# Performance work log

Hardware: AMD Instinct MI355X
Metric: run time of the kernel (lower is better)

Reference implementation:

```python
import jax, jax.numpy as jnp
import numpy as np


def setup_inputs() -> dict:
    key = jax.random.key(0)
    k1, k2 = jax.random.split(key)
    inputs = jax.random.normal(k1, (64, 16, 64, 512), dtype=jnp.float32)
    cluster_centers = jax.random.normal(k2, (64, 512), dtype=jnp.float32) * 0.05
    return {"inputs": inputs, "cluster_centers": cluster_centers}


def reference(inputs, cluster_centers):
    # inputs: (B, H, W, C); cluster_centers: (K, C)
    B, H, W, C = inputs.shape
    K = cluster_centers.shape[0]
    x = inputs.reshape(B, H * W, C)                      # (B, N, C)
    # soft assignments: softmax over K of x @ centers^T
    logits = jnp.einsum('bnc,kc->bnk', x, cluster_centers)
    a = jax.nn.softmax(logits, axis=-1)                  # (B, N, K)
    # VLAD rewritten to avoid (B,N,K,C) residual tensor:
    # sum_n a[b,n,k] * (x[b,n,:] - c[k,:])
    #   = (a^T @ x)[b,k,:] - (sum_n a[b,n,k]) * c[k,:]
    agg = jnp.einsum('bnk,bnc->bkc', a, x)               # (B, K, C)
    a_sum = jnp.sum(a, axis=1)                           # (B, K)
    vlad = agg - a_sum[:, :, None] * cluster_centers[None, :, :]
    vlad = vlad.reshape(B, K * C)
    # tf.nn.l2_normalize: x / sqrt(max(sum(x^2), eps)), eps=1e-12
    norm = jnp.sqrt(jnp.maximum(jnp.sum(vlad * vlad, axis=-1, keepdims=True), 1e-12))
    return vlad / norm
```

## Files before the change

### kernel.cpp

```cpp
#include <hip/hip_runtime.h>
#include <stdint.h>

#define NB 64
#define NN 1024
#define CDIM 512
#define KK 64
#define RS 72

typedef __attribute__((ext_vector_type(4))) float f32x4;
typedef __attribute__((ext_vector_type(8))) short short8;
typedef __attribute__((ext_vector_type(4))) unsigned short u16x4;

__device__ __forceinline__ unsigned short f2bf(float f) {
  unsigned int u = __float_as_uint(f);
  return (unsigned short)((u + 0x7fffu + ((u >> 16) & 1u)) >> 16);
}

__global__ __launch_bounds__(256) void k0_cvt(const float* __restrict__ cc,
                                              unsigned short* __restrict__ ccb) {
  int i = blockIdx.x * 256 + threadIdx.x;
  ccb[i] = f2bf(cc[i]);
}

__global__ __launch_bounds__(256) void k1_assign(const float* __restrict__ x,
    const unsigned short* __restrict__ ccb, unsigned short* __restrict__ a_t,
    float* __restrict__ a_sum) {
  const int b = blockIdx.y;
  const int n0 = blockIdx.x << 6;
  const int tid = threadIdx.x;
  const int w = tid >> 6;
  const int l = tid & 63;
  const int lr = l & 15;
  const int lg = l >> 4;

  __shared__ unsigned short a_sm[KK * 64];

  const float* xr = x + ((size_t)b * NN + n0 + (w << 4) + lr) * CDIM + (lg << 3);
  const unsigned short* cb = ccb + lr * CDIM + (lg << 3);

  f32x4 acc0 = {0.f, 0.f, 0.f, 0.f}, acc1 = acc0, acc2 = acc0, acc3 = acc0;

  #pragma unroll 2
  for (int cs = 0; cs < CDIM; cs += 32) {
    f32x4 xa = *(const f32x4*)(xr + cs);
    f32x4 xb = *(const f32x4*)(xr + cs + 4);
    short8 af;
    af[0] = (short)f2bf(xa[0]); af[1] = (short)f2bf(xa[1]);
    af[2] = (short)f2bf(xa[2]); af[3] = (short)f2bf(xa[3]);
    af[4] = (short)f2bf(xb[0]); af[5] = (short)f2bf(xb[1]);
    af[6] = (short)f2bf(xb[2]); af[7] = (short)f2bf(xb[3]);
    short8 b0 = *(const short8*)(cb + cs);
    short8 b1 = *(const short8*)(cb + 16 * CDIM + cs);
    short8 b2 = *(const short8*)(cb + 32 * CDIM + cs);
    short8 b3 = *(const short8*)(cb + 48 * CDIM + cs);
    acc0 = __builtin_amdgcn_mfma_f32_16x16x32_bf16(af, b0, acc0, 0, 0, 0);
    acc1 = __builtin_amdgcn_mfma_f32_16x16x32_bf16(af, b1, acc1, 0, 0, 0);
    acc2 = __builtin_amdgcn_mfma_f32_16x16x32_bf16(af, b2, acc2, 0, 0, 0);
    acc3 = __builtin_amdgcn_mfma_f32_16x16x32_bf16(af, b3, acc3, 0, 0, 0);
  }

  const int swzb = (lr & 7) << 3;
  float s0 = 0.f, s1 = 0.f, s2 = 0.f, s3 = 0.f;
  #pragma unroll
  for (int j = 0; j < 4; ++j) {
    float m = fmaxf(fmaxf(acc0[j], acc1[j]), fmaxf(acc2[j], acc3[j]));
    m = fmaxf(m, __shfl_xor(m, 1));
    m = fmaxf(m, __shfl_xor(m, 2));
    m = fmaxf(m, __shfl_xor(m, 4));
    m = fmaxf(m, __shfl_xor(m, 8));
    float e0 = __expf(acc0[j] - m);
    float e1 = __expf(acc1[j] - m);
    float e2 = __expf(acc2[j] - m);
    float e3 = __expf(acc3[j] - m);
    float s = e0 + e1 + e2 + e3;
    s += __shfl_xor(s, 1); s += __shfl_xor(s, 2);
    s += __shfl_xor(s, 4); s += __shfl_xor(s, 8);
    float inv = 1.0f / s;
    e0 *= inv; e1 *= inv; e2 *= inv; e3 *= inv;
    int r = (w << 4) + (lg << 2) + j;
    int rs = r ^ swzb;
    a_sm[( lr       << 6) + rs] = f2bf(e0);
    a_sm[((16 + lr) << 6) + rs] = f2bf(e1);
    a_sm[((32 + lr) << 6) + rs] = f2bf(e2);
    a_sm[((48 + lr) << 6) + rs] = f2bf(e3);
    s0 += e0; s1 += e1; s2 += e2; s3 += e3;
  }
  s0 += __shfl_xor(s0, 16); s0 += __shfl_xor(s0, 32);
  s1 += __shfl_xor(s1, 16); s1 += __shfl_xor(s1, 32);
  s2 += __shfl_xor(s2, 16); s2 += __shfl_xor(s2, 32);
  s3 += __shfl_xor(s3, 16); s3 += __shfl_xor(s3, 32);
  if (lg == 0) {
    atomicAdd(&a_sum[(b << 6) + lr],      s0);
    atomicAdd(&a_sum[(b << 6) + 16 + lr], s1);
    atomicAdd(&a_sum[(b << 6) + 32 + lr], s2);
    atomicAdd(&a_sum[(b << 6) + 48 + lr], s3);
  }
  __syncthreads();
  const unsigned int* au = (const unsigned int*)a_sm;
  for (int e = tid; e < 2048; e += 256) {
    int kc = e >> 5, n2 = e & 31;
    unsigned int v = au[(kc << 5) + (n2 ^ ((kc & 7) << 2))];
    *((unsigned int*)(a_t + (((size_t)((b << 6) + kc)) << 10) + n0) + n2) = v;
  }
}

__global__ __launch_bounds__(256, 4) void k2_agg(const float* __restrict__ x,
    const unsigned short* __restrict__ a_t, const float* __restrict__ cc,
    const float* __restrict__ a_sum, float* __restrict__ out,
    float* __restrict__ sumsq) {
  const int b = blockIdx.y;
  const int c0 = blockIdx.x << 7;
  const int tid = threadIdx.x;
  const int w = tid >> 6;
  const int l = tid & 63;
  const int lr = l & 15;
  const int lg = l >> 4;

  __shared__ unsigned short xL[2][128 * RS];
  __shared__ float red[4];

  f32x4 acc[8];
  #pragma unroll
  for (int i = 0; i < 8; ++i) acc[i] = (f32x4){0.f, 0.f, 0.f, 0.f};

  const int cl = tid & 127;
  const int ob = (tid >> 7) << 2;
  const float* xb = x + (size_t)b * NN * CDIM + c0 + cl;
  const unsigned short* ap =
      a_t + (((size_t)((b << 6) + (w << 4) + lr)) << 10) + (lg << 3);

  #pragma unroll
  for (int p = 0; p < 4; ++p) {
    const int nl = (ob + p) << 3;
    const float* xp = xb + (size_t)nl * CDIM;
    short8 pk;
    #pragma unroll
    for (int q = 0; q < 8; ++q) pk[q] = (short)f2bf(xp[(size_t)q * CDIM]);
    *(short8*)&xL[0][cl * RS + nl] = pk;
  }
  short8 a_cur0 = *(const short8*)(ap);
  short8 a_cur1 = *(const short8*)(ap + 32);
  __syncthreads();

  for (int it = 0; it < 16; ++it) {
    const int cur = it & 1;
    float xr[32];
    short8 a_nxt0, a_nxt1;
    if (it < 15) {
      const int n0 = (it + 1) << 6;
      #pragma unroll
      for (int p = 0; p < 4; ++p) {
        const float* xp = xb + (size_t)(n0 + ((ob + p) << 3)) * CDIM;
        #pragma unroll
        for (int q = 0; q < 8; ++q) xr[p * 8 + q] = xp[(size_t)q * CDIM];
      }
      a_nxt0 = *(const short8*)(ap + n0);
      a_nxt1 = *(const short8*)(ap + n0 + 32);
    }
    #pragma unroll
    for (int ns = 0; ns < 64; ns += 32) {
      const short8 af = ns == 0 ? a_cur0 : a_cur1;
      #pragma unroll
      for (int ct = 0; ct < 8; ++ct) {
        const int row = (ct << 4) + lr;
        short8 bf = *(const short8*)&xL[cur][row * RS + ns + (lg << 3)];
        acc[ct] = __builtin_amdgcn_mfma_f32_16x16x32_bf16(af, bf, acc[ct], 0, 0, 0);
      }
    }
    if (it < 15) {
      const int nxt = cur ^ 1;
      #pragma unroll
      for (int p = 0; p < 4; ++p) {
        const int nl = (ob + p) << 3;
        short8 pk;
        #pragma unroll
        for (int q = 0; q < 8; ++q) pk[q] = (short)f2bf(xr[p * 8 + q]);
        *(short8*)&xL[nxt][cl * RS + nl] = pk;
      }
      a_cur0 = a_nxt0;
      a_cur1 = a_nxt1;
    }
    __syncthreads();
  }

  float lsum = 0.f;
  #pragma unroll
  for (int ct = 0; ct < 8; ++ct) {
    #pragma unroll
    for (int j = 0; j < 4; ++j) {
      int k = (w << 4) + (lg << 2) + j;
      int c = c0 + (ct << 4) + lr;
      float v = acc[ct][j] - a_sum[(b << 6) + k] * cc[k * CDIM + c];
      out[((size_t)b << 15) + (k << 9) + c] = v;
      lsum += v * v;
    }
  }
  lsum += __shfl_xor(lsum, 1);  lsum += __shfl_xor(lsum, 2);
  lsum += __shfl_xor(lsum, 4);  lsum += __shfl_xor(lsum, 8);
  lsum += __shfl_xor(lsum, 16); lsum += __shfl_xor(lsum, 32);
  if (l == 0) red[w] = lsum;
  __syncthreads();
  if (tid == 0) atomicAdd(&sumsq[b], red[0] + red[1] + red[2] + red[3]);
}

__global__ __launch_bounds__(256) void k3_norm(float* __restrict__ out,
                                               const float* __restrict__ sumsq) {
  int idx = blockIdx.x * 256 + threadIdx.x;
  int b = idx >> 13;
  float s = sumsq[b];
  float scale = 1.0f / sqrtf(fmaxf(s, 1e-12f));
  f32x4* io = (f32x4*)out;
  f32x4 v = io[idx];
  v[0] *= scale; v[1] *= scale; v[2] *= scale; v[3] *= scale;
  io[idx] = v;
}

extern "C" void kernel_launch(void* const* d_in, const int* in_sizes, int n_in,
                              void* d_out, int out_size, void* d_ws, size_t ws_size,
                              hipStream_t stream) {
  const float* x  = (const float*)d_in[0];
  const float* cc = (const float*)d_in[1];
  float* out = (float*)d_out;
  char* ws = (char*)d_ws;
  unsigned short* a_t = (unsigned short*)ws;
  unsigned short* ccb = (unsigned short*)(ws + (8u << 20));
  float* a_sum = (float*)(ws + (8u << 20) + (64u << 10));
  float* sumsq = a_sum + NB * KK;

  (void)hipMemsetAsync(a_sum, 0, NB * KK * 4 + NB * 4, stream);
  k0_cvt<<<dim3((KK * CDIM) / 256), 256, 0, stream>>>(cc, ccb);
  k1_assign<<<dim3(16, NB), 256, 0, stream>>>(x, ccb, a_t, a_sum);
  k2_agg<<<dim3(4, NB), 256, 0, stream>>>(x, a_t, cc, a_sum, out, sumsq);
  k3_norm<<<dim3(2048), 256, 0, stream>>>(out, sumsq);
}
```

Before: 89.68 us.

## Emit transposed bf16 x from assignment kernel and read it in aggregation

The assignment kernel, which already converts x to bf16 for the logits MFMA, now also transposes those bf16 values through shared memory and writes a C-major packed bf16 copy of x to workspace. The aggregation kernel then reads this half-size pre-transposed copy with coalesced loads instead of re-reading fp32 x with strided column loads and converting it again. The aggregation kernel also switches to 64-channel tiles, doubling its grid, and uses lighter LDS-only barriers. The cost is an extra 32 MB of writes and more LDS and barriers in the assignment kernel.

```diff
diff --git a/kernel.cpp b/kernel.cpp
--- a/kernel.cpp
+++ b/kernel.cpp
@@ -5,15 +5,20 @@
 #define NN 1024
 #define CDIM 512
 #define KK 64
-#define RS 72
+#define XRS 38
 
 typedef __attribute__((ext_vector_type(4))) float f32x4;
 typedef __attribute__((ext_vector_type(8))) short short8;
-typedef __attribute__((ext_vector_type(4))) unsigned short u16x4;
 
 __device__ __forceinline__ unsigned short f2bf(float f) {
   unsigned int u = __float_as_uint(f);
   return (unsigned short)((u + 0x7fffu + ((u >> 16) & 1u)) >> 16);
+}
+
+__device__ __forceinline__ void lgkm_barrier() {
+  asm volatile("s_waitcnt lgkmcnt(0)" ::: "memory");
+  __builtin_amdgcn_sched_barrier(0);
+  __builtin_amdgcn_s_barrier();
 }
 
 __global__ __launch_bounds__(256) void k0_cvt(const float* __restrict__ cc,
@@ -24,7 +29,7 @@
 
 __global__ __launch_bounds__(256) void k1_assign(const float* __restrict__ x,
     const unsigned short* __restrict__ ccb, unsigned short* __restrict__ a_t,
-    float* __restrict__ a_sum) {
+    unsigned int* __restrict__ xT32, float* __restrict__ a_sum) {
   const int b = blockIdx.y;
   const int n0 = blockIdx.x << 6;
   const int tid = threadIdx.x;
@@ -33,15 +38,19 @@
   const int lr = l & 15;
   const int lg = l >> 4;
 
+  __shared__ unsigned int xs[128 * XRS];
   __shared__ unsigned short a_sm[KK * 64];
 
   const float* xr = x + ((size_t)b * NN + n0 + (w << 4) + lr) * CDIM + (lg << 3);
   const unsigned short* cb = ccb + lr * CDIM + (lg << 3);
+  const int n2 = (w << 3) + (lr >> 1);
+  const int codd = l & 1;
 
   f32x4 acc0 = {0.f, 0.f, 0.f, 0.f}, acc1 = acc0, acc2 = acc0, acc3 = acc0;
 
-  #pragma unroll 2
-  for (int cs = 0; cs < CDIM; cs += 32) {
+  #pragma unroll 4
+  for (int i = 0; i < 16; ++i) {
+    const int cs = i << 5;
     f32x4 xa = *(const f32x4*)(xr + cs);
     f32x4 xb = *(const f32x4*)(xr + cs + 4);
     short8 af;
@@ -57,6 +66,33 @@
     acc1 = __builtin_amdgcn_mfma_f32_16x16x32_bf16(af, b1, acc1, 0, 0, 0);
     acc2 = __builtin_amdgcn_mfma_f32_16x16x32_bf16(af, b2, acc2, 0, 0, 0);
     acc3 = __builtin_amdgcn_mfma_f32_16x16x32_bf16(af, b3, acc3, 0, 0, 0);
+
+    {
+      const unsigned int* afu = (const unsigned int*)&af;
+      const int cbase = ((i & 3) << 5) + (lg << 3) + codd;
+      #pragma unroll
+      for (int j = 0; j < 4; ++j) {
+        unsigned int own = afu[j];
+        unsigned int oth = (unsigned int)__shfl_xor((int)own, 1);
+        unsigned int first  = codd ? oth : own;
+        unsigned int second = codd ? own : oth;
+        unsigned int lo = (first & 0xffffu) | (second << 16);
+        unsigned int hi = (first >> 16) | (second & 0xffff0000u);
+        xs[(cbase + (j << 1)) * XRS + n2] = codd ? hi : lo;
+      }
+    }
+    if ((i & 3) == 3) {
+      lgkm_barrier();
+      const int s = i >> 2;
+      const size_t gb = ((size_t)(b << 9) + (s << 7)) << 9;
+      #pragma unroll
+      for (int p = 0; p < 16; ++p) {
+        const int f = (p << 8) + tid;
+        unsigned int v = xs[(f >> 5) * XRS + (f & 31)];
+        xT32[gb + (((size_t)(f >> 5)) << 9) + (n0 >> 1) + (f & 31)] = v;
+      }
+      lgkm_barrier();
+    }
   }
 
   const int swzb = (lr & 7) << 3;
@@ -98,94 +134,85 @@
   __syncthreads();
   const unsigned int* au = (const unsigned int*)a_sm;
   for (int e = tid; e < 2048; e += 256) {
-    int kc = e >> 5, n2 = e & 31;
-    unsigned int v = au[(kc << 5) + (n2 ^ ((kc & 7) << 2))];
-    *((unsigned int*)(a_t + (((size_t)((b << 6) + kc)) << 10) + n0) + n2) = v;
-  }
-}
-
-__global__ __launch_bounds__(256, 4) void k2_agg(const float* __restrict__ x,
-    const unsigned short* __restrict__ a_t, const float* __restrict__ cc,
-    const float* __restrict__ a_sum, float* __restrict__ out,
-    float* __restrict__ sumsq) {
+    int kc = e >> 5, nn2 = e & 31;
+    unsigned int v = au[(kc << 5) + (nn2 ^ ((kc & 7) << 2))];
+    *((unsigned int*)(a_t + (((size_t)((b << 6) + kc)) << 10) + n0) + nn2) = v;
+  }
+}
+
+__global__ __launch_bounds__(256) void k2_agg(
+    const unsigned short* __restrict__ a_t, const unsigned int* __restrict__ xT32,
+    const float* __restrict__ cc, const float* __restrict__ a_sum,
+    float* __restrict__ out, float* __restrict__ sumsq) {
   const int b = blockIdx.y;
-  const int c0 = blockIdx.x << 7;
+  const int c0 = blockIdx.x << 6;
   const int tid = threadIdx.x;
   const int w = tid >> 6;
   const int l = tid & 63;
   const int lr = l & 15;
   const int lg = l >> 4;
 
-  __shared__ unsigned short xL[2][128 * RS];
+  __shared__ unsigned int xs[2][64 * XRS];
   __shared__ float red[4];
 
-  f32x4 acc[8];
-  #pragma unroll
-  for (int i = 0; i < 8; ++i) acc[i] = (f32x4){0.f, 0.f, 0.f, 0.f};
-
-  const int cl = tid & 127;
-  const int ob = (tid >> 7) << 2;
-  const float* xb = x + (size_t)b * NN * CDIM + c0 + cl;
+  f32x4 acc[4];
+  #pragma unroll
+  for (int i = 0; i < 4; ++i) acc[i] = (f32x4){0.f, 0.f, 0.f, 0.f};
+
   const unsigned short* ap =
       a_t + (((size_t)((b << 6) + (w << 4) + lr)) << 10) + (lg << 3);
-
-  #pragma unroll
-  for (int p = 0; p < 4; ++p) {
-    const int nl = (ob + p) << 3;
-    const float* xp = xb + (size_t)nl * CDIM;
-    short8 pk;
-    #pragma unroll
-    for (int q = 0; q < 8; ++q) pk[q] = (short)f2bf(xp[(size_t)q * CDIM]);
-    *(short8*)&xL[0][cl * RS + nl] = pk;
+  const unsigned int* xg =
+      xT32 + (((size_t)((b << 9) + c0 + (tid >> 5))) << 9) + (tid & 31);
+
+  #pragma unroll
+  for (int p = 0; p < 8; ++p) {
+    const int f = (p << 8) + tid;
+    xs[0][(f >> 5) * XRS + (f & 31)] = xg[(((size_t)p) << 12)];
   }
   short8 a_cur0 = *(const short8*)(ap);
   short8 a_cur1 = *(const short8*)(ap + 32);
-  __syncthreads();
+  lgkm_barrier();
 
   for (int it = 0; it < 16; ++it) {
     const int cur = it & 1;
-    float xr[32];
+    unsigned int xr[8];
     short8 a_nxt0, a_nxt1;
     if (it < 15) {
-      const int n0 = (it + 1) << 6;
-      #pragma unroll
-      for (int p = 0; p < 4; ++p) {
-        const float* xp = xb + (size_t)(n0 + ((ob + p) << 3)) * CDIM;
-        #pragma unroll
-        for (int q = 0; q < 8; ++q) xr[p * 8 + q] = xp[(size_t)q * CDIM];
-      }
-      a_nxt0 = *(const short8*)(ap + n0);
-      a_nxt1 = *(const short8*)(ap + n0 + 32);
+      const int nu = (it + 1) << 5;
+      #pragma unroll
+      for (int p = 0; p < 8; ++p) xr[p] = xg[(((size_t)p) << 12) + nu];
+      a_nxt0 = *(const short8*)(ap + ((it + 1) << 6));
+      a_nxt1 = *(const short8*)(ap + ((it + 1) << 6) + 32);
     }
     #pragma unroll
     for (int ns = 0; ns < 64; ns += 32) {
       const short8 af = ns == 0 ? a_cur0 : a_cur1;
       #pragma unroll
-      for (int ct = 0; ct < 8; ++ct) {
+      for (int ct = 0; ct < 4; ++ct) {
         const int row = (ct << 4) + lr;
-        short8 bf = *(const short8*)&xL[cur][row * RS + ns + (lg << 3)];
-        acc[ct] = __builtin_amdgcn_mfma_f32_16x16x32_bf16(af, bf, acc[ct], 0, 0, 0);
+        const unsigned long long* bp = (const unsigned long long*)
+            &xs[cur][row * XRS + (ns >> 1) + (lg << 2)];
+        union { unsigned long long q[2]; short8 s; } u;
+        u.q[0] = bp[0];
+        u.q[1] = bp[1];
+        acc[ct] = __builtin_amdgcn_mfma_f32_16x16x32_bf16(af, u.s, acc[ct], 0, 0, 0);
       }
     }
     if (it < 15) {
-      const int nxt = cur ^ 1;
-      #pragma unroll
-      for (int p = 0; p < 4; ++p) {
-        const int nl = (ob + p) << 3;
-        short8 pk;
-        #pragma unroll
-        for (int q = 0; q < 8; ++q) pk[q] = (short)f2bf(xr[p * 8 + q]);
-        *(short8*)&xL[nxt][cl * RS + nl] = pk;
+      #pragma unroll
+      for (int p = 0; p < 8; ++p) {
+        const int f = (p << 8) + tid;
+        xs[cur ^ 1][(f >> 5) * XRS + (f & 31)] = xr[p];
       }
       a_cur0 = a_nxt0;
       a_cur1 = a_nxt1;
     }
-    __syncthreads();
+    lgkm_barrier();
   }
 
   float lsum = 0.f;
   #pragma unroll
-  for (int ct = 0; ct < 8; ++ct) {
+  for (int ct = 0; ct < 4; ++ct) {
     #pragma unroll
     for (int j = 0; j < 4; ++j) {
       int k = (w << 4) + (lg << 2) + j;
@@ -226,10 +253,11 @@
   unsigned short* ccb = (unsigned short*)(ws + (8u << 20));
   float* a_sum = (float*)(ws + (8u << 20) + (64u << 10));
   float* sumsq = a_sum + NB * KK;
+  unsigned int* xT32 = (unsigned int*)(ws + (16u << 20));
 
   (void)hipMemsetAsync(a_sum, 0, NB * KK * 4 + NB * 4, stream);
   k0_cvt<<<dim3((KK * CDIM) / 256), 256, 0, stream>>>(cc, ccb);
-  k1_assign<<<dim3(16, NB), 256, 0, stream>>>(x, ccb, a_t, a_sum);
-  k2_agg<<<dim3(4, NB), 256, 0, stream>>>(x, a_t, cc, a_sum, out, sumsq);
+  k1_assign<<<dim3(16, NB), 256, 0, stream>>>(x, ccb, a_t, xT32, a_sum);
+  k2_agg<<<dim3(8, NB), 256, 0, stream>>>(a_t, xT32, cc, a_sum, out, sumsq);
   k3_norm<<<dim3(2048), 256, 0, stream>>>(out, sumsq);
 }
```

New measurement: 89.90 us. No clear change (+0.2%).
